# Optimization experiments

Measured on AMD Instinct MI355X. Metric: run time of the kernel, lower is better.

The kernel has to match this reference:

```python
import jax, jax.numpy as jnp
import numpy as np

MULT_CLASS = 6  # int(1/0.2) + 1
EPS = 1e-4


def setup_inputs() -> dict:
    key = jax.random.key(0)
    ks = jax.random.split(key, 8)
    bs, C, M, D = 16384, 10000, MULT_CLASS, 256
    return {
        "data": jax.random.normal(ks[0], (bs, D), dtype=jnp.float32),
        "source_labels": jax.random.randint(ks[1], (bs,), 0, C, dtype=jnp.int32),
        "beta": jax.random.uniform(ks[2], (bs,), dtype=jnp.float32),
        "centers": jax.random.normal(ks[3], (C * M, D), dtype=jnp.float32),
        "W1": jax.random.normal(ks[4], (M, C), dtype=jnp.float32) * 0.02,
        "b1": jnp.zeros((M,), dtype=jnp.float32),
        "W2": jax.random.normal(ks[5], (M, M), dtype=jnp.float32) * 0.1,
        "b2": jnp.zeros((M,), dtype=jnp.float32),
        "memory": jnp.zeros((C * M, D), dtype=jnp.float32),
        "memory_weights": jnp.zeros((C * M, 1), dtype=jnp.float32),
    }


def _weights_from_hotmatrix(beta, labels, W1, b1, W2, b2):
    # LSM(one_hot(label)) : one_hot @ W1.T == gather of W1 columns (same math,
    # avoids materializing the [bs, num_classes] one-hot matrix)
    h = jax.nn.relu(W1.T[labels] + b1)            # [bs, M]
    out = jax.nn.sigmoid(h @ W2.T + b2) + EPS      # [bs, M]
    column_sum = jnp.cumsum(out, axis=1)           # [bs, M]
    val = (beta[:, None] - column_sum) ** 2
    w = jnp.exp(-jnp.sqrt(val + 1e-10))
    norm_w = w / (jnp.sum(w, axis=1, keepdims=True) + EPS + 1e-10)
    return norm_w, column_sum


def reference(data, source_labels, beta, centers, W1, b1, W2, b2, memory, memory_weights):
    bs, D = data.shape
    M = W1.shape[0]
    C = W1.shape[1]
    norm_w, sum_v = _weights_from_hotmatrix(beta, source_labels, W1, b1, W2, b2)

    # --- get_MSML_loss: label-indexed gather of a contiguous center block,
    # per-row weighting, reduce over the block ---
    centers3 = centers.reshape(C, M, D)
    centers_lab = centers3[source_labels]                      # [bs, M, D]
    center_matrix = jnp.einsum("bmd,bm->bd", centers_lab, norm_w)
    loss = jnp.mean((data - center_matrix) ** 2)

    # --- update_center: scatter-add weighted features into memory banks ---
    feat_cent = data[:, None, :] * norm_w[:, :, None]          # [bs, M, D]
    new_memory = memory.reshape(C, M, D).at[source_labels].add(feat_cent)
    new_memory_w = memory_weights.reshape(C, M).at[source_labels].add(norm_w)
    return (loss, sum_v, new_memory.reshape(C * M, D), new_memory_w.reshape(C * M, 1))
```

## Files before the change

kernel.cpp:

```cpp
#include <hip/hip_runtime.h>

constexpr int kBS = 16384;
constexpr int kC  = 10000;
constexpr int kM  = 6;
constexpr int kD  = 256;
constexpr float kEPS = 1e-4f;

__global__ __launch_bounds__(256) void k_hist(
    const int* __restrict__ labels, int* counts, int* __restrict__ rank,
    float* loss_out)
{
    const int row = blockIdx.x * 256 + threadIdx.x;
    if (row == 0) *loss_out = 0.f;
    if (row < kBS) rank[row] = atomicAdd(counts + labels[row], 1);
}

__global__ __launch_bounds__(1024) void k_scan(
    const int* __restrict__ counts, int* __restrict__ starts)
{
    __shared__ int part[1024];
    const int t = threadIdx.x;
    const int base = t * 10;
    int local[10];
    int s = 0;
#pragma unroll
    for (int i = 0; i < 10; ++i) {
        const int idx = base + i;
        const int c = (idx < kC) ? counts[idx] : 0;
        local[i] = s; s += c;
    }
    part[t] = s;
    __syncthreads();
    for (int off = 1; off < 1024; off <<= 1) {
        const int v = part[t];
        const int add = (t >= off) ? part[t - off] : 0;
        __syncthreads();
        part[t] = v + add;
        __syncthreads();
    }
    const int excl = part[t] - s;
#pragma unroll
    for (int i = 0; i < 10; ++i) {
        const int idx = base + i;
        if (idx < kC) starts[idx] = excl + local[i];
    }
    if (t == 1023) starts[kC] = excl + s;
}

__global__ __launch_bounds__(256) void k_place(
    const int* __restrict__ labels, const int* __restrict__ rank,
    const int* __restrict__ starts, int* __restrict__ order)
{
    const int row = blockIdx.x * 256 + threadIdx.x;
    if (row < kBS) order[starts[labels[row]] + rank[row]] = row;
}

__global__ __launch_bounds__(256) void k_agg(
    const float* __restrict__ data,
    const float* __restrict__ beta,
    const int*   __restrict__ starts,
    const int*   __restrict__ order,
    const float* __restrict__ W1,
    const float* __restrict__ b1,
    const float* __restrict__ W2,
    const float* __restrict__ b2,
    const float* __restrict__ centers,
    const float* __restrict__ memory,
    const float* __restrict__ memw,
    float*       loss_out,
    float* __restrict__ sum_v,
    float* __restrict__ mem_out,
    float* __restrict__ mw_out)
{
    __shared__ float ls[4];
    const int wid  = threadIdx.x >> 6;
    const int lane = threadIdx.x & 63;
    const int lab  = blockIdx.x * 4 + wid;

    const size_t cbase = (size_t)lab * (kM * kD);

    const int s0 = starts[lab];
    const int s1 = starts[lab + 1];

    float4 acc[kM];
    float  mwacc[kM];
#pragma unroll
    for (int m = 0; m < kM; ++m) {
        acc[m] = make_float4(0.f, 0.f, 0.f, 0.f);
        mwacc[m] = 0.f;
    }
    float lossacc = 0.f;

    if (s1 > s0) {
        float4 cv[kM];
#pragma unroll
        for (int m = 0; m < kM; ++m)
            cv[m] = ((const float4*)(centers + cbase + (size_t)m * kD))[lane];

        float csarr[kM];
        {
            float h[kM];
#pragma unroll
            for (int m = 0; m < kM; ++m) {
                float v = W1[m * kC + lab] + b1[m];
                h[m] = v > 0.f ? v : 0.f;
            }
            float cs = 0.f;
#pragma unroll
            for (int m = 0; m < kM; ++m) {
                float z = b2[m];
#pragma unroll
                for (int j = 0; j < kM; ++j) z += W2[m * kM + j] * h[j];
                cs += 1.f / (1.f + expf(-z)) + kEPS;
                csarr[m] = cs;
            }
        }
        float csel = csarr[0];
        csel = (lane == 1) ? csarr[1] : csel;
        csel = (lane == 2) ? csarr[2] : csel;
        csel = (lane == 3) ? csarr[3] : csel;
        csel = (lane == 4) ? csarr[4] : csel;
        csel = (lane == 5) ? csarr[5] : csel;

        int p = s0;
        while (p < s1) {
            const int bc = min(4, s1 - p);
            int rows[4];
#pragma unroll
            for (int i = 0; i < 4; ++i) if (i < bc) rows[i] = order[p + i];
            float4 dv[4];
            float  bet[4];
#pragma unroll
            for (int i = 0; i < 4; ++i) if (i < bc) {
                dv[i]  = ((const float4*)(data + (size_t)rows[i] * kD))[lane];
                bet[i] = beta[rows[i]];
            }
#pragma unroll
            for (int i = 0; i < 4; ++i) if (i < bc) {
                float nw[kM];
                float wsum = 0.f;
#pragma unroll
                for (int m = 0; m < kM; ++m) {
                    const float dvb = bet[i] - csarr[m];
                    const float wv = expf(-sqrtf(dvb * dvb + 1e-10f));
                    nw[m] = wv;
                    wsum += wv;
                }
                const float inv = 1.f / (wsum + kEPS + 1e-10f);
                float4 cm = make_float4(0.f, 0.f, 0.f, 0.f);
#pragma unroll
                for (int m = 0; m < kM; ++m) {
                    const float w = nw[m] * inv;
                    cm.x += w * cv[m].x; cm.y += w * cv[m].y;
                    cm.z += w * cv[m].z; cm.w += w * cv[m].w;
                    acc[m].x += w * dv[i].x; acc[m].y += w * dv[i].y;
                    acc[m].z += w * dv[i].z; acc[m].w += w * dv[i].w;
                    mwacc[m] += w;
                }
                const float ax = dv[i].x - cm.x, ay = dv[i].y - cm.y;
                const float az = dv[i].z - cm.z, aw = dv[i].w - cm.w;
                lossacc += ax * ax + ay * ay + az * az + aw * aw;
                if (lane < kM) sum_v[rows[i] * kM + lane] = csel;
            }
            p += bc;
        }
    }

    float4 mv[kM];
#pragma unroll
    for (int m = 0; m < kM; ++m)
        mv[m] = ((const float4*)(memory + cbase + (size_t)m * kD))[lane];
    const float mwold = (lane < kM) ? memw[(size_t)lab * kM + lane] : 0.f;

#pragma unroll
    for (int m = 0; m < kM; ++m) {
        float4 o;
        o.x = mv[m].x + acc[m].x; o.y = mv[m].y + acc[m].y;
        o.z = mv[m].z + acc[m].z; o.w = mv[m].w + acc[m].w;
        ((float4*)(mem_out + cbase + (size_t)m * kD))[lane] = o;
    }
    float msel = mwacc[0];
    msel = (lane == 1) ? mwacc[1] : msel;
    msel = (lane == 2) ? mwacc[2] : msel;
    msel = (lane == 3) ? mwacc[3] : msel;
    msel = (lane == 4) ? mwacc[4] : msel;
    msel = (lane == 5) ? mwacc[5] : msel;
    if (lane < kM) mw_out[(size_t)lab * kM + lane] = mwold + msel;

#pragma unroll
    for (int off = 32; off > 0; off >>= 1) lossacc += __shfl_down(lossacc, off, 64);
    if (lane == 0) ls[wid] = lossacc;
    __syncthreads();
    if (threadIdx.x == 0) {
        const float s = ls[0] + ls[1] + ls[2] + ls[3];
        atomicAdd(loss_out, s * (1.f / ((float)kBS * (float)kD)));
    }
}

extern "C" void kernel_launch(void* const* d_in, const int* in_sizes, int n_in,
                              void* d_out, int out_size, void* d_ws, size_t ws_size,
                              hipStream_t stream) {
    const float* data    = (const float*)d_in[0];
    const int*   labels  = (const int*)  d_in[1];
    const float* beta    = (const float*)d_in[2];
    const float* centers = (const float*)d_in[3];
    const float* W1      = (const float*)d_in[4];
    const float* b1      = (const float*)d_in[5];
    const float* W2      = (const float*)d_in[6];
    const float* b2      = (const float*)d_in[7];
    const float* memory  = (const float*)d_in[8];
    const float* memw    = (const float*)d_in[9];

    float* out     = (float*)d_out;
    float* loss    = out;
    float* sum_v   = out + 1;
    float* mem_out = out + 1 + (size_t)kBS * kM;
    float* mw_out  = mem_out + (size_t)kC * kM * kD;

    int* counts = (int*)d_ws;
    int* starts = counts + kC;
    int* rank   = starts + kC + 1;
    int* order  = rank + kBS;

    hipMemsetAsync(counts, 0, kC * sizeof(int), stream);

    k_hist<<<dim3((kBS + 255) / 256), dim3(256), 0, stream>>>(
        labels, counts, rank, loss);

    k_scan<<<dim3(1), dim3(1024), 0, stream>>>(counts, starts);

    k_place<<<dim3((kBS + 255) / 256), dim3(256), 0, stream>>>(
        labels, rank, starts, order);

    k_agg<<<dim3(kC / 4), dim3(256), 0, stream>>>(
        data, beta, starts, order, W1, b1, W2, b2,
        centers, memory, memw, loss, sum_v, mem_out, mw_out);
}
```

Baseline: 215.8 us.

## Use wave-shuffle scan and replace loss atomics with per-label partials plus final reduce

The single-block scan changes from a shared-memory Hillis-Steele loop with many block barriers to a wave-level shuffle scan followed by a small cross-wave scan. The loss reduction stops issuing a global float atomicAdd from each aggregation block and instead writes one partial per label, which a new single-block kernel sums deterministically. This removes barrier and atomic overhead but adds one extra kernel launch.

```diff
diff --git a/kernel.cpp b/kernel.cpp
--- a/kernel.cpp
+++ b/kernel.cpp
@@ -7,19 +7,19 @@
 constexpr float kEPS = 1e-4f;
 
 __global__ __launch_bounds__(256) void k_hist(
-    const int* __restrict__ labels, int* counts, int* __restrict__ rank,
-    float* loss_out)
+    const int* __restrict__ labels, int* counts, int* __restrict__ rank)
 {
     const int row = blockIdx.x * 256 + threadIdx.x;
-    if (row == 0) *loss_out = 0.f;
     if (row < kBS) rank[row] = atomicAdd(counts + labels[row], 1);
 }
 
 __global__ __launch_bounds__(1024) void k_scan(
     const int* __restrict__ counts, int* __restrict__ starts)
 {
-    __shared__ int part[1024];
-    const int t = threadIdx.x;
+    __shared__ int wtot[16];
+    const int t    = threadIdx.x;
+    const int lane = t & 63;
+    const int wid  = t >> 6;
     const int base = t * 10;
     int local[10];
     int s = 0;
@@ -29,16 +29,26 @@
         const int c = (idx < kC) ? counts[idx] : 0;
         local[i] = s; s += c;
     }
-    part[t] = s;
+    int inc = s;
+#pragma unroll
+    for (int off = 1; off < 64; off <<= 1) {
+        const int v = __shfl_up(inc, off, 64);
+        if (lane >= off) inc += v;
+    }
+    if (lane == 63) wtot[wid] = inc;
     __syncthreads();
-    for (int off = 1; off < 1024; off <<= 1) {
-        const int v = part[t];
-        const int add = (t >= off) ? part[t - off] : 0;
-        __syncthreads();
-        part[t] = v + add;
-        __syncthreads();
-    }
-    const int excl = part[t] - s;
+    if (wid == 0) {
+        int v = (lane < 16) ? wtot[lane] : 0;
+        int vi = v;
+#pragma unroll
+        for (int off = 1; off < 16; off <<= 1) {
+            const int u = __shfl_up(vi, off, 64);
+            if (lane >= off) vi += u;
+        }
+        if (lane < 16) wtot[lane] = vi - v;
+    }
+    __syncthreads();
+    const int excl = (inc - s) + wtot[wid];
 #pragma unroll
     for (int i = 0; i < 10; ++i) {
         const int idx = base + i;
@@ -67,12 +77,11 @@
     const float* __restrict__ centers,
     const float* __restrict__ memory,
     const float* __restrict__ memw,
-    float*       loss_out,
+    float* __restrict__ partial,
     float* __restrict__ sum_v,
     float* __restrict__ mem_out,
     float* __restrict__ mw_out)
 {
-    __shared__ float ls[4];
     const int wid  = threadIdx.x >> 6;
     const int lane = threadIdx.x & 63;
     const int lab  = blockIdx.x * 4 + wid;
@@ -189,12 +198,24 @@
 
 #pragma unroll
     for (int off = 32; off > 0; off >>= 1) lossacc += __shfl_down(lossacc, off, 64);
-    if (lane == 0) ls[wid] = lossacc;
+    if (lane == 0) partial[lab] = lossacc;
+}
+
+__global__ __launch_bounds__(256) void k_final(
+    const float* __restrict__ partial, float* __restrict__ loss_out)
+{
+    __shared__ float ls[4];
+    const int t    = threadIdx.x;
+    const int lane = t & 63;
+    const int wid  = t >> 6;
+    float s = 0.f;
+    for (int i = t; i < kC; i += 256) s += partial[i];
+#pragma unroll
+    for (int off = 32; off > 0; off >>= 1) s += __shfl_down(s, off, 64);
+    if (lane == 0) ls[wid] = s;
     __syncthreads();
-    if (threadIdx.x == 0) {
-        const float s = ls[0] + ls[1] + ls[2] + ls[3];
-        atomicAdd(loss_out, s * (1.f / ((float)kBS * (float)kD)));
-    }
+    if (t == 0)
+        *loss_out = (ls[0] + ls[1] + ls[2] + ls[3]) * (1.f / ((float)kBS * (float)kD));
 }
 
 extern "C" void kernel_launch(void* const* d_in, const int* in_sizes, int n_in,
@@ -217,22 +238,21 @@
     float* mem_out = out + 1 + (size_t)kBS * kM;
     float* mw_out  = mem_out + (size_t)kC * kM * kD;
 
-    int* counts = (int*)d_ws;
-    int* starts = counts + kC;
-    int* rank   = starts + kC + 1;
-    int* order  = rank + kBS;
+    int*   counts  = (int*)d_ws;
+    int*   starts  = counts + kC;
+    int*   rank    = starts + kC + 1;
+    int*   order   = rank + kBS;
+    float* partial = (float*)(order + kBS);
 
     hipMemsetAsync(counts, 0, kC * sizeof(int), stream);
 
-    k_hist<<<dim3((kBS + 255) / 256), dim3(256), 0, stream>>>(
-        labels, counts, rank, loss);
-
+    k_hist<<<dim3((kBS + 255) / 256), dim3(256), 0, stream>>>(labels, counts, rank);
     k_scan<<<dim3(1), dim3(1024), 0, stream>>>(counts, starts);
-
-    k_place<<<dim3((kBS + 255) / 256), dim3(256), 0, stream>>>(
-        labels, rank, starts, order);
+    k_place<<<dim3((kBS + 255) / 256), dim3(256), 0, stream>>>(labels, rank, starts, order);
 
     k_agg<<<dim3(kC / 4), dim3(256), 0, stream>>>(
         data, beta, starts, order, W1, b1, W2, b2,
-        centers, memory, memw, loss, sum_v, mem_out, mw_out);
-}
+        centers, memory, memw, partial, sum_v, mem_out, mw_out);
+
+    k_final<<<dim3(1), dim3(256), 0, stream>>>(partial, loss);
+}
```

Measured after the change: 220.6 us. 1.02x slower.
